# Performance work log

Measured on AMD Instinct MI355X. Metric: run time of the kernel, lower is better.

Reference implementation:

```python
import jax, jax.numpy as jnp
import numpy as np

LN_EPS = 1e-5   # torch nn.LayerNorm default
OPM_EPS = 1e-3  # module eps


def _layer_norm(x, gamma, beta):
    mu = jnp.mean(x, axis=-1, keepdims=True)
    var = jnp.var(x, axis=-1, keepdims=True)
    return (x - mu) * jax.lax.rsqrt(var + LN_EPS) * gamma + beta


def setup_inputs() -> dict:
    key = jax.random.key(0)
    ks = jax.random.split(key, 4)
    S, N, c_m, c_h, c_z = 128, 384, 256, 32, 128
    return {
        "m": jax.random.normal(ks[0], (S, N, c_m), dtype=jnp.float32),
        "mask": jnp.ones((S, N), dtype=jnp.float32),
        "ln_gamma": jnp.ones((c_m,), dtype=jnp.float32),
        "ln_beta": jnp.zeros((c_m,), dtype=jnp.float32),
        "w1": jax.random.normal(ks[1], (c_m, c_h), dtype=jnp.float32) / np.sqrt(c_m),
        "b1": jnp.zeros((c_h,), dtype=jnp.float32),
        "w2": jax.random.normal(ks[2], (c_m, c_h), dtype=jnp.float32) / np.sqrt(c_m),
        "b2": jnp.zeros((c_h,), dtype=jnp.float32),
        "w_out": jax.random.normal(ks[3], (c_h * c_h, c_z), dtype=jnp.float32) / np.sqrt(c_h * c_h),
        "b_out": jnp.zeros((c_z,), dtype=jnp.float32),
    }


def reference(m, mask, ln_gamma, ln_beta, w1, b1, w2, b2, w_out, b_out):
    # m: [S, N, C_m], mask: [S, N]
    ln = _layer_norm(m, ln_gamma, ln_beta)                      # [S, N, C_m]
    a = (ln @ w1 + b1) * mask[..., None]                        # [S, N, C_h]
    b = (ln @ w2 + b2) * mask[..., None]                        # [S, N, C_h]
    a = jnp.swapaxes(a, -2, -3)                                 # [N, S, C_h]
    b = jnp.swapaxes(b, -2, -3)                                 # [N, S, C_h]
    norm = jnp.einsum('si,sj->ij', mask, mask)[..., None] + OPM_EPS  # [N, N, 1]
    outer = jnp.einsum('isc,jsd->ijcd', a, b)                   # [N, N, C_h, C_h]
    outer = outer.reshape(outer.shape[:-2] + (-1,))             # [N, N, C_h^2]
    out = outer @ w_out + b_out                                 # [N, N, C_z]
    return out / norm
```

## Files before the change

### kernel.cpp

```cpp
#include <hip/hip_runtime.h>
#include <hip/hip_bf16.h>

#define S_ 128
#define N_ 384
#define CM 256
#define CH 32
#define CZ 128

typedef __attribute__((ext_vector_type(8))) __bf16 bf16x8;
typedef __attribute__((ext_vector_type(4))) float f32x4;

union pack4 { __hip_bfloat16 h[4]; uint2 u; };

__global__ __launch_bounds__(256) void k_w12(const float* __restrict__ w1,
                                             const float* __restrict__ w2,
                                             __hip_bfloat16* __restrict__ wt12)
{
    const int ncol = blockIdx.x, t = threadIdx.x;
    const float* w = (ncol < CH) ? w1 : w2;
    wt12[ncol * CM + t] = __float2bfloat16(w[(size_t)t * CH + (ncol & 31)]);
}

__global__ __launch_bounds__(256) void k_wt(const float* __restrict__ wout,
                                            __hip_bfloat16* __restrict__ woutT)
{
    const int z = blockIdx.x;
    for (int cd = threadIdx.x; cd < CH*CH; cd += 256)
        woutT[(size_t)z * (CH*CH) + cd] = __float2bfloat16(wout[(size_t)cd * CZ + z]);
}

__global__ __launch_bounds__(N_) void k_rnorm(const float* __restrict__ mask,
                                              float* __restrict__ RN)
{
    const int i = blockIdx.x, j = threadIdx.x;
    float acc = 0.f;
    #pragma unroll 8
    for (int s = 0; s < S_; ++s)
        acc += mask[s*N_ + i] * mask[s*N_ + j];
    RN[i*N_ + j] = 1.0f / (acc + 1e-3f);
}

#define LNR 264
__global__ __launch_bounds__(256) void k_lnp(
    const float* __restrict__ m, const float* __restrict__ mask,
    const float* __restrict__ gamma, const float* __restrict__ beta,
    const float* __restrict__ b1, const float* __restrict__ b2,
    const __hip_bfloat16* __restrict__ wt12,
    __hip_bfloat16* __restrict__ At, __hip_bfloat16* __restrict__ Bt)
{
    __shared__ __hip_bfloat16 lnS[128 * LNR];
    __shared__ float msk[128];
    const int n0 = blockIdx.x * 16, s0 = blockIdx.y * 8;
    const int t = threadIdx.x, wave = t >> 6, lane = t & 63;
    const int l15 = lane & 15, quad = lane >> 4;

    if (t < 128) msk[t] = mask[(s0 + (t & 7))*N_ + n0 + (t >> 3)];

    float4 g  = ((const float4*)gamma)[lane];
    float4 be = ((const float4*)beta)[lane];
    for (int i = 0; i < 32; ++i) {
        const int row = wave*32 + i;
        const int n = row >> 3, s = row & 7;
        float4 x = ((const float4*)(m + ((size_t)((s0+s)*N_ + n0 + n)) * CM))[lane];
        float sum = x.x + x.y + x.z + x.w;
        float ssq = x.x*x.x + x.y*x.y + x.z*x.z + x.w*x.w;
        #pragma unroll
        for (int off = 32; off >= 1; off >>= 1) {
            sum += __shfl_xor(sum, off, 64);
            ssq += __shfl_xor(ssq, off, 64);
        }
        const float mean = sum * (1.0f/CM);
        const float var  = ssq * (1.0f/CM) - mean*mean;
        const float rstd = rsqrtf(var + 1e-5f);
        pack4 pk;
        pk.h[0] = __float2bfloat16((x.x - mean)*rstd*g.x + be.x);
        pk.h[1] = __float2bfloat16((x.y - mean)*rstd*g.y + be.y);
        pk.h[2] = __float2bfloat16((x.z - mean)*rstd*g.z + be.z);
        pk.h[3] = __float2bfloat16((x.w - mean)*rstd*g.w + be.w);
        *(uint2*)&lnS[row*LNR + lane*4] = pk.u;
    }
    __syncthreads();

    f32x4 acc[2][4];
    const f32x4 z4 = {0.f,0.f,0.f,0.f};
    #pragma unroll
    for (int mt = 0; mt < 2; ++mt)
        #pragma unroll
        for (int nt = 0; nt < 4; ++nt) acc[mt][nt] = z4;

    #pragma unroll
    for (int kk = 0; kk < 8; ++kk) {
        bf16x8 a0 = *(const bf16x8*)&lnS[(wave*32      + l15)*LNR + kk*32 + quad*8];
        bf16x8 a1 = *(const bf16x8*)&lnS[(wave*32 + 16 + l15)*LNR + kk*32 + quad*8];
        #pragma unroll
        for (int nt = 0; nt < 4; ++nt) {
            bf16x8 wv = *(const bf16x8*)&wt12[(size_t)(nt*16 + l15)*CM + kk*32 + quad*8];
            acc[0][nt] = __builtin_amdgcn_mfma_f32_16x16x32_bf16(a0, wv, acc[0][nt], 0,0,0);
            acc[1][nt] = __builtin_amdgcn_mfma_f32_16x16x32_bf16(a1, wv, acc[1][nt], 0,0,0);
        }
    }

    #pragma unroll
    for (int nt = 0; nt < 4; ++nt) {
        const int ncol = nt*16 + l15;
        const int sel = ncol >> 5, c = ncol & 31;
        const float bias = sel ? b2[c] : b1[c];
        __hip_bfloat16* dst = sel ? Bt : At;
        #pragma unroll
        for (int mt = 0; mt < 2; ++mt) {
            const int rowb = wave*32 + mt*16 + quad*4;
            const int n_loc = rowb >> 3, s_loc = rowb & 7;
            pack4 pk;
            #pragma unroll
            for (int r = 0; r < 4; ++r)
                pk.h[r] = __float2bfloat16((acc[mt][nt][r] + bias) * msk[rowb + r]);
            *(uint2*)&dst[((size_t)(n0 + n_loc)*CH + c)*S_ + s0 + s_loc] = pk.u;
        }
    }
}

#define OR 1160
__global__ __launch_bounds__(512) void k_opm(
    const __hip_bfloat16* __restrict__ At, const __hip_bfloat16* __restrict__ Bt,
    const float* __restrict__ RN, const __hip_bfloat16* __restrict__ woutT,
    const float* __restrict__ bout, float* __restrict__ out)
{
    __shared__ __hip_bfloat16 O[64 * OR];
    const int t = threadIdx.x;
    const int wave = t >> 6, lane = t & 63;
    const int l15 = lane & 15, quad = lane >> 4;
    const int i0 = blockIdx.x * 8, j0 = blockIdx.y * 8;
    const int mhalf = wave & 1, nquad = wave >> 1;

    f32x4 acc[4][8];
    const f32x4 z4 = {0.f,0.f,0.f,0.f};
    #pragma unroll
    for (int nt = 0; nt < 4; ++nt)
        #pragma unroll
        for (int mt = 0; mt < 8; ++mt) acc[nt][mt] = z4;

    const __hip_bfloat16* Ag[8];
    #pragma unroll
    for (int mt = 0; mt < 8; ++mt) {
        const int Mrow = mhalf*128 + mt*16 + l15;
        Ag[mt] = At + ((size_t)(i0 + (Mrow >> 5)) * CH + (Mrow & 31)) * S_ + quad*8;
    }
    const __hip_bfloat16* Bg[4];
    #pragma unroll
    for (int nt = 0; nt < 4; ++nt) {
        const int Ncol = nquad*64 + nt*16 + l15;
        Bg[nt] = Bt + ((size_t)(j0 + (Ncol >> 5)) * CH + (Ncol & 31)) * S_ + quad*8;
    }

    #pragma unroll
    for (int kk = 0; kk < 4; ++kk) {
        bf16x8 af[8], bfr[4];
        #pragma unroll
        for (int mt = 0; mt < 8; ++mt) af[mt] = *(const bf16x8*)(Ag[mt] + kk*32);
        #pragma unroll
        for (int nt = 0; nt < 4; ++nt) bfr[nt] = *(const bf16x8*)(Bg[nt] + kk*32);
        #pragma unroll
        for (int nt = 0; nt < 4; ++nt)
            #pragma unroll
            for (int mt = 0; mt < 8; ++mt)
                acc[nt][mt] = __builtin_amdgcn_mfma_f32_16x16x32_bf16(
                    bfr[nt], af[mt], acc[nt][mt], 0, 0, 0);
    }

    #pragma unroll
    for (int mt = 0; mt < 8; ++mt) {
        const int Mcol = mhalf*128 + mt*16 + l15;
        const int i_l = Mcol >> 5, c = Mcol & 31;
        #pragma unroll
        for (int nt = 0; nt < 4; ++nt) {
            const int Nrow = nquad*64 + nt*16 + quad*4;
            const int j_l = Nrow >> 5, d0 = Nrow & 31;
            const int p = i_l*8 + j_l;
            pack4 pk;
            #pragma unroll
            for (int r = 0; r < 4; ++r) pk.h[r] = __float2bfloat16(acc[nt][mt][r]);
            *(uint2*)&O[p*OR + c*36 + d0] = pk.u;
        }
    }
    __syncthreads();

    const int zb = wave * 16;
    bf16x8 wf[32];
    #pragma unroll
    for (int kk = 0; kk < 32; ++kk)
        wf[kk] = *(const bf16x8*)&woutT[(size_t)(zb + l15) * (CH*CH) + kk*32 + quad*8];

    f32x4 oacc[4];
    #pragma unroll
    for (int mt = 0; mt < 4; ++mt) oacc[mt] = z4;

    #pragma unroll
    for (int kk = 0; kk < 32; ++kk) {
        #pragma unroll
        for (int mt = 0; mt < 4; ++mt) {
            bf16x8 a = *(const bf16x8*)&O[(mt*16 + l15)*OR + kk*36 + quad*8];
            oacc[mt] = __builtin_amdgcn_mfma_f32_16x16x32_bf16(a, wf[kk], oacc[mt], 0,0,0);
        }
    }

    const int zc = zb + l15;
    const float bz = bout[zc];
    #pragma unroll
    for (int mt = 0; mt < 4; ++mt) {
        #pragma unroll
        for (int r = 0; r < 4; ++r) {
            const int p = mt*16 + quad*4 + r;
            const int i = i0 + (p >> 3), j = j0 + (p & 7);
            const float rn = RN[i*N_ + j];
            out[((size_t)(i*N_ + j))*CZ + zc] = (oacc[mt][r] + bz) * rn;
        }
    }
}

extern "C" void kernel_launch(void* const* d_in, const int* in_sizes, int n_in,
                              void* d_out, int out_size, void* d_ws, size_t ws_size,
                              hipStream_t stream)
{
    const float* m    = (const float*)d_in[0];
    const float* mask = (const float*)d_in[1];
    const float* gam  = (const float*)d_in[2];
    const float* bet  = (const float*)d_in[3];
    const float* w1   = (const float*)d_in[4];
    const float* b1   = (const float*)d_in[5];
    const float* w2   = (const float*)d_in[6];
    const float* b2   = (const float*)d_in[7];
    const float* wout = (const float*)d_in[8];
    const float* bout = (const float*)d_in[9];
    float* out = (float*)d_out;

    __hip_bfloat16* At    = (__hip_bfloat16*)d_ws;
    __hip_bfloat16* Bt    = At + (size_t)N_ * CH * S_;
    __hip_bfloat16* woutT = Bt + (size_t)N_ * CH * S_;
    __hip_bfloat16* wt12  = woutT + (size_t)CZ * CH * CH;
    float*          RN    = (float*)(wt12 + (size_t)64 * CM);

    k_w12<<<64, 256, 0, stream>>>(w1, w2, wt12);
    k_wt<<<CZ, 256, 0, stream>>>(wout, woutT);
    k_rnorm<<<N_, N_, 0, stream>>>(mask, RN);
    dim3 gl(24, 16);
    k_lnp<<<gl, 256, 0, stream>>>(m, mask, gam, bet, b1, b2, wt12, At, Bt);
    dim3 grid(N_ / 8, N_ / 8);
    k_opm<<<grid, 512, 0, stream>>>(At, Bt, RN, woutT, bout, out);
}
```

Baseline: 332.1 us.

## Make outer-product kernel persistent, fuse norm computation, swizzle LDS, merge prep kernels

The outer-product kernel becomes persistent: 256 blocks each loop over 18 smaller 8x4 (i,j) tiles. Each block loads its slice of the transposed w_out into registers once and reuses it across all its tiles. The mask-normalisation kernel is removed, and each tile now computes its reciprocal norm in-kernel with a shuffle reduction. The LDS staging buffer uses an XOR swizzle in place of padding, stores use nontemporal hints, and the two weight-prep kernels are merged into one launch. This cuts launch count and w_out reloads, at the cost of smaller MFMA tiles, two barriers per tile and repeated mask reads.

```diff
diff --git a/kernel.cpp b/kernel.cpp
--- a/kernel.cpp
+++ b/kernel.cpp
@@ -12,32 +12,21 @@
 
 union pack4 { __hip_bfloat16 h[4]; uint2 u; };
 
-__global__ __launch_bounds__(256) void k_w12(const float* __restrict__ w1,
-                                             const float* __restrict__ w2,
-                                             __hip_bfloat16* __restrict__ wt12)
-{
-    const int ncol = blockIdx.x, t = threadIdx.x;
-    const float* w = (ncol < CH) ? w1 : w2;
-    wt12[ncol * CM + t] = __float2bfloat16(w[(size_t)t * CH + (ncol & 31)]);
-}
-
-__global__ __launch_bounds__(256) void k_wt(const float* __restrict__ wout,
-                                            __hip_bfloat16* __restrict__ woutT)
-{
-    const int z = blockIdx.x;
-    for (int cd = threadIdx.x; cd < CH*CH; cd += 256)
-        woutT[(size_t)z * (CH*CH) + cd] = __float2bfloat16(wout[(size_t)cd * CZ + z]);
-}
-
-__global__ __launch_bounds__(N_) void k_rnorm(const float* __restrict__ mask,
-                                              float* __restrict__ RN)
-{
-    const int i = blockIdx.x, j = threadIdx.x;
-    float acc = 0.f;
-    #pragma unroll 8
-    for (int s = 0; s < S_; ++s)
-        acc += mask[s*N_ + i] * mask[s*N_ + j];
-    RN[i*N_ + j] = 1.0f / (acc + 1e-3f);
+__global__ __launch_bounds__(256) void k_prep(const float* __restrict__ w1,
+                                              const float* __restrict__ w2,
+                                              const float* __restrict__ wout,
+                                              __hip_bfloat16* __restrict__ wt12,
+                                              __hip_bfloat16* __restrict__ woutT)
+{
+    const int b = blockIdx.x, t = threadIdx.x;
+    if (b < 64) {
+        const float* w = (b < CH) ? w1 : w2;
+        wt12[b * CM + t] = __float2bfloat16(w[(size_t)t * CH + (b & 31)]);
+    } else {
+        const int z = b - 64;
+        for (int cd = t; cd < CH*CH; cd += 256)
+            woutT[(size_t)z * (CH*CH) + cd] = __float2bfloat16(wout[(size_t)cd * CZ + z]);
+    }
 }
 
 #define LNR 264
@@ -119,101 +108,124 @@
     }
 }
 
-#define OR 1160
-__global__ __launch_bounds__(512) void k_opm(
+__global__ __launch_bounds__(512, 2) void k_opm(
     const __hip_bfloat16* __restrict__ At, const __hip_bfloat16* __restrict__ Bt,
-    const float* __restrict__ RN, const __hip_bfloat16* __restrict__ woutT,
+    const float* __restrict__ mask, const __hip_bfloat16* __restrict__ woutT,
     const float* __restrict__ bout, float* __restrict__ out)
 {
-    __shared__ __hip_bfloat16 O[64 * OR];
+    __shared__ __hip_bfloat16 O[32 * 1024];
+    __shared__ float RNl[32];
     const int t = threadIdx.x;
     const int wave = t >> 6, lane = t & 63;
     const int l15 = lane & 15, quad = lane >> 4;
-    const int i0 = blockIdx.x * 8, j0 = blockIdx.y * 8;
-    const int mhalf = wave & 1, nquad = wave >> 1;
-
-    f32x4 acc[4][8];
-    const f32x4 z4 = {0.f,0.f,0.f,0.f};
-    #pragma unroll
-    for (int nt = 0; nt < 4; ++nt)
-        #pragma unroll
-        for (int mt = 0; mt < 8; ++mt) acc[nt][mt] = z4;
-
-    const __hip_bfloat16* Ag[8];
-    #pragma unroll
-    for (int mt = 0; mt < 8; ++mt) {
-        const int Mrow = mhalf*128 + mt*16 + l15;
-        Ag[mt] = At + ((size_t)(i0 + (Mrow >> 5)) * CH + (Mrow & 31)) * S_ + quad*8;
-    }
-    const __hip_bfloat16* Bg[4];
-    #pragma unroll
-    for (int nt = 0; nt < 4; ++nt) {
-        const int Ncol = nquad*64 + nt*16 + l15;
-        Bg[nt] = Bt + ((size_t)(j0 + (Ncol >> 5)) * CH + (Ncol & 31)) * S_ + quad*8;
-    }
-
-    #pragma unroll
-    for (int kk = 0; kk < 4; ++kk) {
-        bf16x8 af[8], bfr[4];
-        #pragma unroll
-        for (int mt = 0; mt < 8; ++mt) af[mt] = *(const bf16x8*)(Ag[mt] + kk*32);
-        #pragma unroll
-        for (int nt = 0; nt < 4; ++nt) bfr[nt] = *(const bf16x8*)(Bg[nt] + kk*32);
-        #pragma unroll
-        for (int nt = 0; nt < 4; ++nt)
-            #pragma unroll
-            for (int mt = 0; mt < 8; ++mt)
-                acc[nt][mt] = __builtin_amdgcn_mfma_f32_16x16x32_bf16(
-                    bfr[nt], af[mt], acc[nt][mt], 0, 0, 0);
-    }
-
-    #pragma unroll
-    for (int mt = 0; mt < 8; ++mt) {
-        const int Mcol = mhalf*128 + mt*16 + l15;
-        const int i_l = Mcol >> 5, c = Mcol & 31;
-        #pragma unroll
-        for (int nt = 0; nt < 4; ++nt) {
-            const int Nrow = nquad*64 + nt*16 + quad*4;
-            const int j_l = Nrow >> 5, d0 = Nrow & 31;
-            const int p = i_l*8 + j_l;
-            pack4 pk;
-            #pragma unroll
-            for (int r = 0; r < 4; ++r) pk.h[r] = __float2bfloat16(acc[nt][mt][r]);
-            *(uint2*)&O[p*OR + c*36 + d0] = pk.u;
-        }
-    }
-    __syncthreads();
+    const int mq = wave & 3, nh = wave >> 2;
 
     const int zb = wave * 16;
     bf16x8 wf[32];
     #pragma unroll
     for (int kk = 0; kk < 32; ++kk)
         wf[kk] = *(const bf16x8*)&woutT[(size_t)(zb + l15) * (CH*CH) + kk*32 + quad*8];
-
-    f32x4 oacc[4];
-    #pragma unroll
-    for (int mt = 0; mt < 4; ++mt) oacc[mt] = z4;
-
-    #pragma unroll
-    for (int kk = 0; kk < 32; ++kk) {
+    const float bz = bout[zb + l15];
+
+    const f32x4 z4 = {0.f,0.f,0.f,0.f};
+
+    for (int tl = 0; tl < 18; ++tl) {
+        const int tile = blockIdx.x * 18 + tl;
+        const int i0 = (tile / 96) * 8, j0 = (tile % 96) * 4;
+
+        f32x4 acc[4][4];
+        #pragma unroll
+        for (int nt = 0; nt < 4; ++nt)
+            #pragma unroll
+            for (int mt = 0; mt < 4; ++mt) acc[nt][mt] = z4;
+
+        int aOff[4], bOff[4];
         #pragma unroll
         for (int mt = 0; mt < 4; ++mt) {
-            bf16x8 a = *(const bf16x8*)&O[(mt*16 + l15)*OR + kk*36 + quad*8];
-            oacc[mt] = __builtin_amdgcn_mfma_f32_16x16x32_bf16(a, wf[kk], oacc[mt], 0,0,0);
-        }
-    }
-
-    const int zc = zb + l15;
-    const float bz = bout[zc];
-    #pragma unroll
-    for (int mt = 0; mt < 4; ++mt) {
-        #pragma unroll
-        for (int r = 0; r < 4; ++r) {
-            const int p = mt*16 + quad*4 + r;
-            const int i = i0 + (p >> 3), j = j0 + (p & 7);
-            const float rn = RN[i*N_ + j];
-            out[((size_t)(i*N_ + j))*CZ + zc] = (oacc[mt][r] + bz) * rn;
-        }
+            const int Mrow = mq*64 + mt*16 + l15;
+            aOff[mt] = ((i0 + (Mrow >> 5)) * CH + (Mrow & 31)) * S_ + quad*8;
+        }
+        #pragma unroll
+        for (int nt = 0; nt < 4; ++nt) {
+            const int Ncol = nh*64 + nt*16 + l15;
+            bOff[nt] = ((j0 + (Ncol >> 5)) * CH + (Ncol & 31)) * S_ + quad*8;
+        }
+
+        #pragma unroll
+        for (int kk = 0; kk < 4; ++kk) {
+            bf16x8 af[4], bfr[4];
+            #pragma unroll
+            for (int mt = 0; mt < 4; ++mt) af[mt]  = *(const bf16x8*)&At[aOff[mt] + kk*32];
+            #pragma unroll
+            for (int nt = 0; nt < 4; ++nt) bfr[nt] = *(const bf16x8*)&Bt[bOff[nt] + kk*32];
+            #pragma unroll
+            for (int nt = 0; nt < 4; ++nt)
+                #pragma unroll
+                for (int mt = 0; mt < 4; ++mt)
+                    acc[nt][mt] = __builtin_amdgcn_mfma_f32_16x16x32_bf16(
+                        bfr[nt], af[mt], acc[nt][mt], 0, 0, 0);
+        }
+
+        {
+            const int p = wave*4 + quad;
+            const int ic = i0 + (p >> 2), jc = j0 + (p & 3);
+            float a = 0.f;
+            #pragma unroll
+            for (int u = 0; u < 8; ++u) {
+                const int s = l15*8 + u;
+                a += mask[s*N_ + ic] * mask[s*N_ + jc];
+            }
+            a += __shfl_xor(a, 1, 64);
+            a += __shfl_xor(a, 2, 64);
+            a += __shfl_xor(a, 4, 64);
+            a += __shfl_xor(a, 8, 64);
+            if (l15 == 0) RNl[p] = 1.0f / (a + 1e-3f);
+        }
+
+        #pragma unroll
+        for (int mt = 0; mt < 4; ++mt) {
+            const int Mcol = mq*64 + mt*16 + l15;
+            const int i_l = Mcol >> 5, c = Mcol & 31;
+            #pragma unroll
+            for (int nt = 0; nt < 4; ++nt) {
+                const int Nrow = nh*64 + nt*16 + quad*4;
+                const int j_l = Nrow >> 5, d0 = Nrow & 31;
+                const int p = i_l*4 + j_l;
+                pack4 pk;
+                #pragma unroll
+                for (int r = 0; r < 4; ++r) pk.h[r] = __float2bfloat16(acc[nt][mt][r]);
+                const int idx = p*1024 + (d0 >> 3)*256 + ((c ^ (p & 7)) << 3)
+                              + ((d0 >> 2) & 1)*4;
+                *(uint2*)&O[idx] = pk.u;
+            }
+        }
+        __syncthreads();
+
+        f32x4 oacc[2];
+        oacc[0] = z4; oacc[1] = z4;
+        #pragma unroll
+        for (int kk = 0; kk < 32; ++kk) {
+            #pragma unroll
+            for (int mt2 = 0; mt2 < 2; ++mt2) {
+                const int row = mt2*16 + l15;
+                bf16x8 a = *(const bf16x8*)&O[row*1024 + quad*256
+                                              + ((kk ^ (row & 7)) << 3)];
+                oacc[mt2] = __builtin_amdgcn_mfma_f32_16x16x32_bf16(
+                    a, wf[kk], oacc[mt2], 0, 0, 0);
+            }
+        }
+
+        #pragma unroll
+        for (int mt2 = 0; mt2 < 2; ++mt2) {
+            #pragma unroll
+            for (int r = 0; r < 4; ++r) {
+                const int p = mt2*16 + quad*4 + r;
+                const int i = i0 + (p >> 2), j = j0 + (p & 3);
+                __builtin_nontemporal_store((oacc[mt2][r] + bz) * RNl[p],
+                    &out[((size_t)(i*N_ + j))*CZ + zb + l15]);
+            }
+        }
+        __syncthreads();
     }
 }
 
@@ -237,13 +249,9 @@
     __hip_bfloat16* Bt    = At + (size_t)N_ * CH * S_;
     __hip_bfloat16* woutT = Bt + (size_t)N_ * CH * S_;
     __hip_bfloat16* wt12  = woutT + (size_t)CZ * CH * CH;
-    float*          RN    = (float*)(wt12 + (size_t)64 * CM);
-
-    k_w12<<<64, 256, 0, stream>>>(w1, w2, wt12);
-    k_wt<<<CZ, 256, 0, stream>>>(wout, woutT);
-    k_rnorm<<<N_, N_, 0, stream>>>(mask, RN);
+
+    k_prep<<<192, 256, 0, stream>>>(w1, w2, wout, wt12, woutT);
     dim3 gl(24, 16);
     k_lnp<<<gl, 256, 0, stream>>>(m, mask, gam, bet, b1, b2, wt12, At, Bt);
-    dim3 grid(N_ / 8, N_ / 8);
-    k_opm<<<grid, 512, 0, stream>>>(At, Bt, RN, woutT, bout, out);
-}
+    k_opm<<<256, 512, 0, stream>>>(At, Bt, mask, woutT, bout, out);
+}
```

After: 493.4 us. 48.6% more time.
